# Optimization experiments

Hardware: AMD Instinct MI355X
Metric: run time of the kernel (lower is better)

## Reference

```python
import jax, jax.numpy as jnp
import numpy as np

D_MODEL = 256   # dim // 2
DIM = 512
D_INNER = 512   # expand=2 * d_model
D_STATE = 16
D_CONV = 4
DT_RANK = 16    # ceil(d_model/16)
N_LAYERS = 2
H_RES, W_RES = 16, 16
EPS = 1e-5


def silu(v):
    return v * jax.nn.sigmoid(v)


def setup_inputs() -> dict:
    key = jax.random.key(0)
    ks = jax.random.split(key, 12)
    Bsz, T, N = 2, 4, 256
    x = jax.random.normal(ks[0], (Bsz, 1 + T * N, DIM), jnp.float32)
    skip = jax.random.normal(ks[1], (Bsz, 1 + 4 * T * N, D_MODEL), jnp.float32)
    sc = lambda k, shape, s: jax.random.normal(k, shape, jnp.float32) * s
    exp_w = sc(ks[2], (2 * DIM, DIM), 0.02)            # PatchExpanding2D.expansion (no bias)
    ln_g = jnp.ones((DIM // 2,), jnp.float32)
    ln_b = jnp.zeros((DIM // 2,), jnp.float32)
    cls_w = sc(ks[3], (DIM // 2, DIM), 0.02)
    cls_b = jnp.zeros((DIM // 2,), jnp.float32)
    in_proj_w = sc(ks[4], (N_LAYERS, 2 * D_INNER, D_MODEL), 0.02)
    conv_w = sc(ks[5], (N_LAYERS, D_INNER, D_CONV), 0.1)  # depthwise causal conv
    conv_b = jnp.zeros((N_LAYERS, D_INNER), jnp.float32)
    xproj_w = sc(ks[6], (N_LAYERS, DT_RANK + 2 * D_STATE, D_INNER), 0.02)
    dt_w = sc(ks[7], (N_LAYERS, D_INNER, DT_RANK), 0.1)
    dt_b = sc(ks[8], (N_LAYERS, D_INNER), 0.1)
    A_log = jnp.log(jnp.broadcast_to(jnp.arange(1, D_STATE + 1, dtype=jnp.float32), (N_LAYERS, D_INNER, D_STATE)))
    Dp = jnp.ones((N_LAYERS, D_INNER), jnp.float32)
    out_w = sc(ks[9], (N_LAYERS, D_MODEL, D_INNER), 0.02)
    bn_g = jnp.ones((D_MODEL,), jnp.float32)
    bn_b = jnp.zeros((D_MODEL,), jnp.float32)
    return {"x": x, "skip_connection": skip, "exp_w": exp_w, "ln_g": ln_g, "ln_b": ln_b,
            "cls_w": cls_w, "cls_b": cls_b, "in_proj_w": in_proj_w, "conv_w": conv_w,
            "conv_b": conv_b, "xproj_w": xproj_w, "dt_w": dt_w, "dt_b": dt_b,
            "A_log": A_log, "Dp": Dp, "out_w": out_w, "bn_g": bn_g, "bn_b": bn_b,
            "B": 2, "T": 4, "N": 256}


def mamba_layer(u, Wi, cw, cb, Wx, Wdt, bdt, A_log, Dd, Wo):
    # u: [B, L, d_model]
    Bb, L, _ = u.shape
    xz = jnp.einsum('bld,ed->ble', u, Wi)            # [B, L, 2*d_inner]
    xi, z = jnp.split(xz, 2, axis=-1)
    # depthwise causal conv1d (pad left d_conv-1)
    xp = jnp.pad(xi, ((0, 0), (D_CONV - 1, 0), (0, 0)))
    xc = cb + sum(cw[:, k] * xp[:, k:k + L, :] for k in range(D_CONV))
    xi = silu(xc)
    dbc = jnp.einsum('bld,ed->ble', xi, Wx)          # [B, L, dt_rank + 2*d_state]
    dt = dbc[..., :DT_RANK]
    Bm = dbc[..., DT_RANK:DT_RANK + D_STATE]
    Cm = dbc[..., DT_RANK + D_STATE:]
    delta = jax.nn.softplus(jnp.einsum('blr,dr->bld', dt, Wdt) + bdt)  # [B, L, d_inner]
    A = -jnp.exp(A_log)                              # [d_inner, d_state]

    def step(h, inp):
        d_t, B_t, C_t, x_t = inp                     # [B,d], [B,n], [B,n], [B,d]
        h = h * jnp.exp(d_t[..., None] * A) + d_t[..., None] * B_t[:, None, :] * x_t[..., None]
        y = jnp.einsum('bdn,bn->bd', h, C_t)
        return h, y

    h0 = jnp.zeros((Bb, D_INNER, D_STATE), u.dtype)
    xs = (jnp.swapaxes(delta, 0, 1), jnp.swapaxes(Bm, 0, 1),
          jnp.swapaxes(Cm, 0, 1), jnp.swapaxes(xi, 0, 1))
    _, ys = jax.lax.scan(step, h0, xs)               # ys: [L, B, d_inner]
    y = jnp.swapaxes(ys, 0, 1) + xi * Dd
    y = y * silu(z)
    return jnp.einsum('bld,od->blo', y, Wo)          # [B, L, d_model]


def reference(x, skip_connection, exp_w, ln_g, ln_b, cls_w, cls_b, in_proj_w, conv_w,
              conv_b, xproj_w, dt_w, dt_b, A_log, Dp, out_w, bn_g, bn_b, B, T, N):
    cls = x[:B, :1, :]                               # [B, 1, dim]
    toks = x[:, 1:, :].reshape(x.shape[0], T, N, DIM)
    # patch expanding: Linear dim -> 2*dim, then 2x2 pixel shuffle, LayerNorm(dim//2)
    e = jnp.einsum('btnm,em->btne', toks, exp_w)     # [B, T, N, 2*dim]
    m = (2 * DIM) // 4                               # dim // 2
    e = e.reshape(-1, T, H_RES, W_RES, 2, 2, m)
    e = jnp.transpose(e, (0, 1, 2, 4, 3, 5, 6)).reshape(-1, T, 4 * N, m)
    mu = e.mean(-1, keepdims=True)
    var = e.var(-1, keepdims=True)
    e = (e - mu) / jnp.sqrt(var + EPS) * ln_g + ln_b
    e = e.reshape(e.shape[0], T * 4 * N, m)
    cls = jnp.einsum('bom,em->boe', cls, cls_w) + cls_b
    xx = jnp.concatenate([cls, e], axis=1) + skip_connection
    for i in range(N_LAYERS):
        xx = mamba_layer(xx, in_proj_w[i], conv_w[i], conv_b[i], xproj_w[i],
                         dt_w[i], dt_b[i], A_log[i], Dp[i], out_w[i])
    # BatchNorm1d over channels (training-mode batch stats, biased variance)
    mu = xx.mean(axis=(0, 1))
    var = xx.var(axis=(0, 1))
    xx = (xx - mu) / jnp.sqrt(var + EPS) * bn_g + bn_b
    return xx, 4 * N
```

## Files before the change

kernel.cpp:

```cpp
#include <hip/hip_runtime.h>
#include <hip/hip_bf16.h>
#include <math.h>

#define L_TOT 4097
#define BSZ 2
#define ROWS (BSZ*L_TOT)
#define NSEG 128
#define SEGLEN 33

typedef __bf16 bf16x8 __attribute__((ext_vector_type(8)));
typedef float  f32x4  __attribute__((ext_vector_type(4)));
#define ASTR 56

__device__ __forceinline__ float sigmoidf_(float v){ return 1.0f/(1.0f+__expf(-v)); }
__device__ __forceinline__ float siluf_(float v){ return v * sigmoidf_(v); }
__device__ __forceinline__ unsigned short bfbits(float f){
    __bf16 h = (__bf16)f;
    return __builtin_bit_cast(unsigned short, h);
}

__global__ __launch_bounds__(256) void cvt4(
    const float* __restrict__ w0, const float* __restrict__ w1,
    const float* __restrict__ w2, const float* __restrict__ w3,
    __bf16* __restrict__ o0, __bf16* __restrict__ o1,
    __bf16* __restrict__ o2, __bf16* __restrict__ o3)
{
    long i = ((long)blockIdx.x*256 + threadIdx.x)*8;
    const float* src; __bf16* dst; long off;
    if (i < 524288)        { src = w0; dst = o0; off = i; }
    else if (i < 1048576)  { src = w1; dst = o1; off = i - 524288; }
    else if (i < 1310720)  { src = w2; dst = o2; off = i - 1048576; }
    else if (i < 1359872)  { src = w3; dst = o3; off = i - 1310720; }
    else return;
    float4 a = *(const float4*)(src+off), b = *(const float4*)(src+off+4);
    bf16x8 o;
    o[0]=(__bf16)a.x; o[1]=(__bf16)a.y; o[2]=(__bf16)a.z; o[3]=(__bf16)a.w;
    o[4]=(__bf16)b.x; o[5]=(__bf16)b.y; o[6]=(__bf16)b.z; o[7]=(__bf16)b.w;
    *(bf16x8*)(dst+off) = o;
}

__global__ __launch_bounds__(256) void cvt_gather_x(
    const float* __restrict__ x, __bf16* __restrict__ out)
{
    long i = ((long)blockIdx.x*256 + threadIdx.x)*8;
    if (i >= 2048L*512) return;
    int row = (int)(i >> 9), col = (int)(i & 511);
    long srow = row + (row >> 10) + 1;
    const float* src = x + srow*512 + col;
    float4 a = *(const float4*)src, b = *(const float4*)(src+4);
    bf16x8 o;
    o[0]=(__bf16)a.x; o[1]=(__bf16)a.y; o[2]=(__bf16)a.z; o[3]=(__bf16)a.w;
    o[4]=(__bf16)b.x; o[5]=(__bf16)b.y; o[6]=(__bf16)b.z; o[7]=(__bf16)b.w;
    *(bf16x8*)(out+i) = o;
}

template<int SMODE>
__global__ __launch_bounds__(256) void gemm_bf16(
    const __bf16* __restrict__ A, const __bf16* __restrict__ W,
    float* __restrict__ C, __bf16* __restrict__ C2, int M, int N, int K)
{
    __shared__ __bf16 Als[128*ASTR];
    __shared__ __bf16 Wls[64*ASTR];
    const int tid = threadIdx.x;
    const int lane = tid & 63, w = tid >> 6;
    const int n0 = blockIdx.x*64, m0 = blockIdx.y*128;

    f32x4 zero = {0.f,0.f,0.f,0.f};
    f32x4 acc[2][4];
    #pragma unroll
    for (int i=0;i<2;i++)
        #pragma unroll
        for (int j=0;j<4;j++) acc[i][j] = zero;

    const int arow = tid >> 1, ahalf = tid & 1;
    const int wrow = tid >> 2, wseg = tid & 3;
    const int fr = lane & 15, fc = lane >> 4;

    for (int k0 = 0; k0 < K; k0 += 32) {
        bf16x8 av0 = {}, av1 = {};
        if (m0 + arow < M) {
            const __bf16* src = A + (long)(m0+arow)*K + k0 + ahalf*16;
            av0 = *(const bf16x8*)src;
            av1 = *(const bf16x8*)(src+8);
        }
        bf16x8 wv = *(const bf16x8*)(W + (long)(n0+wrow)*K + k0 + wseg*8);
        __syncthreads();
        *(bf16x8*)&Als[arow*ASTR + ahalf*16]     = av0;
        *(bf16x8*)&Als[arow*ASTR + ahalf*16 + 8] = av1;
        *(bf16x8*)&Wls[wrow*ASTR + wseg*8]       = wv;
        __syncthreads();

        bf16x8 a0 = *(const bf16x8*)&Als[(w*32 +      fr)*ASTR + fc*8];
        bf16x8 a1 = *(const bf16x8*)&Als[(w*32 + 16 + fr)*ASTR + fc*8];
        #pragma unroll
        for (int j = 0; j < 4; j++) {
            bf16x8 bv = *(const bf16x8*)&Wls[(j*16 + fr)*ASTR + fc*8];
            acc[0][j] = __builtin_amdgcn_mfma_f32_16x16x32_bf16(a0, bv, acc[0][j], 0,0,0);
            acc[1][j] = __builtin_amdgcn_mfma_f32_16x16x32_bf16(a1, bv, acc[1][j], 0,0,0);
        }
    }
    #pragma unroll
    for (int i = 0; i < 2; i++) {
        #pragma unroll
        for (int rr = 0; rr < 4; rr++) {
            int grow = m0 + w*32 + i*16 + fc*4 + rr;
            if (grow < M) {
                #pragma unroll
                for (int j = 0; j < 4; j++) {
                    float v = acc[i][j][rr];
                    long o = (long)grow*N + n0 + j*16 + fr;
                    if (SMODE != 2) C[o] = v;
                    if (SMODE != 0) C2[o] = (__bf16)v;
                }
            }
        }
    }
}

__global__ __launch_bounds__(128) void gemm_dbc(
    const __bf16* __restrict__ A, const __bf16* __restrict__ W,
    float* __restrict__ C, int M)
{
    __shared__ __bf16 Als[64*ASTR];
    __shared__ __bf16 Wls[48*ASTR];
    const int tid = threadIdx.x;
    const int lane = tid & 63, w = tid >> 6;
    const int m0 = blockIdx.x*64;
    f32x4 zero = {0.f,0.f,0.f,0.f};
    f32x4 acc[2][3];
    #pragma unroll
    for (int i=0;i<2;i++)
        #pragma unroll
        for (int j=0;j<3;j++) acc[i][j] = zero;

    const int arow = tid >> 1, ahalf = tid & 1;
    const int fr = lane & 15, fc = lane >> 4;

    for (int k0 = 0; k0 < 512; k0 += 32) {
        bf16x8 av0 = {}, av1 = {};
        if (m0 + arow < M) {
            const __bf16* src = A + (long)(m0+arow)*512 + k0 + ahalf*16;
            av0 = *(const bf16x8*)src;
            av1 = *(const bf16x8*)(src+8);
        }
        bf16x8 wv0 = {}, wv1 = {};
        if (tid < 96) {
            const __bf16* src = W + (long)(tid>>1)*512 + k0 + (tid&1)*16;
            wv0 = *(const bf16x8*)src;
            wv1 = *(const bf16x8*)(src+8);
        }
        __syncthreads();
        *(bf16x8*)&Als[arow*ASTR + ahalf*16]     = av0;
        *(bf16x8*)&Als[arow*ASTR + ahalf*16 + 8] = av1;
        if (tid < 96) {
            *(bf16x8*)&Wls[(tid>>1)*ASTR + (tid&1)*16]     = wv0;
            *(bf16x8*)&Wls[(tid>>1)*ASTR + (tid&1)*16 + 8] = wv1;
        }
        __syncthreads();

        bf16x8 a0 = *(const bf16x8*)&Als[(w*32 +      fr)*ASTR + fc*8];
        bf16x8 a1 = *(const bf16x8*)&Als[(w*32 + 16 + fr)*ASTR + fc*8];
        #pragma unroll
        for (int j = 0; j < 3; j++) {
            bf16x8 bv = *(const bf16x8*)&Wls[(j*16 + fr)*ASTR + fc*8];
            acc[0][j] = __builtin_amdgcn_mfma_f32_16x16x32_bf16(a0, bv, acc[0][j], 0,0,0);
            acc[1][j] = __builtin_amdgcn_mfma_f32_16x16x32_bf16(a1, bv, acc[1][j], 0,0,0);
        }
    }
    #pragma unroll
    for (int i = 0; i < 2; i++) {
        #pragma unroll
        for (int rr = 0; rr < 4; rr++) {
            int grow = m0 + w*32 + i*16 + fc*4 + rr;
            if (grow < M) {
                #pragma unroll
                for (int j = 0; j < 3; j++)
                    C[(long)grow*48 + j*16 + fr] = acc[i][j][rr];
            }
        }
    }
}

__global__ __launch_bounds__(256) void delta_k(
    const float* __restrict__ dbc, const float* __restrict__ Wdt,
    const float* __restrict__ bdt, const __bf16* __restrict__ xib,
    unsigned* __restrict__ pdx)
{
    const int d0 = threadIdx.x, d1 = threadIdx.x + 256;
    const int r0 = blockIdx.x*8;
    f32x4 wa[4], wb[4];
    #pragma unroll
    for (int q = 0; q < 4; q++) {
        wa[q] = *(const f32x4*)(Wdt + d0*16 + q*4);
        wb[q] = *(const f32x4*)(Wdt + d1*16 + q*4);
    }
    const float b0 = bdt[d0], b1 = bdt[d1];
    #pragma unroll
    for (int rr = 0; rr < 8; rr++) {
        int row = r0 + rr;
        if (row >= ROWS) return;
        const f32x4* p = (const f32x4*)(dbc + (long)row*48);
        f32x4 t0 = p[0], t1 = p[1], t2 = p[2], t3 = p[3];
        float s0 = b0, s1 = b1;
        #pragma unroll
        for (int e = 0; e < 4; e++) {
            s0 += wa[0][e]*t0[e] + wa[1][e]*t1[e] + wa[2][e]*t2[e] + wa[3][e]*t3[e];
            s1 += wb[0][e]*t0[e] + wb[1][e]*t1[e] + wb[2][e]*t2[e] + wb[3][e]*t3[e];
        }
        float dl0 = (s0 > 20.f) ? s0 : log1pf(__expf(s0));
        float dl1 = (s1 > 20.f) ? s1 : log1pf(__expf(s1));
        unsigned x0 = __builtin_bit_cast(unsigned short, xib[(long)row*512 + d0]);
        unsigned x1 = __builtin_bit_cast(unsigned short, xib[(long)row*512 + d1]);
        pdx[(long)row*512 + d0] = (unsigned)bfbits(dl0) | (x0 << 16);
        pdx[(long)row*512 + d1] = (unsigned)bfbits(dl1) | (x1 << 16);
    }
}

__global__ __launch_bounds__(256) void rearrange_ln_cls(
    const __bf16* __restrict__ e_buf, const float* __restrict__ x,
    const float* __restrict__ cls_w, const float* __restrict__ cls_b,
    const float* __restrict__ ln_g, const float* __restrict__ ln_b,
    const float* __restrict__ skip, float* __restrict__ xx,
    __bf16* __restrict__ xxb)
{
    const int blk = blockIdx.x;
    const int b = blk / L_TOT;
    const int q = blk % L_TOT;
    const int c = threadIdx.x;

    if (q == 0) {
        __shared__ float xr[512];
        const float* xrow = x + (long)b*1025*512;
        xr[c] = xrow[c]; xr[c+256] = xrow[c+256];
        __syncthreads();
        float acc = cls_b[c];
        const float4* wrow = (const float4*)(cls_w + (long)c*512);
        #pragma unroll 8
        for (int m4 = 0; m4 < 128; m4++) {
            float4 wv = wrow[m4];
            float4 xv = *(const float4*)&xr[m4*4];
            acc += wv.x*xv.x + wv.y*xv.y + wv.z*xv.z + wv.w*xv.w;
        }
        long o = (long)b*L_TOT*256 + c;
        float v = acc + skip[o];
        xx[o] = v; xxb[o] = (__bf16)v;
        return;
    }
    const int t  = (q-1) >> 10;
    const int p  = (q-1) & 1023;
    const int h  = p >> 6;
    const int a  = (p >> 5) & 1;
    const int w  = (p >> 1) & 15;
    const int bb = p & 1;
    const long tok = (long)b*1024 + t*256 + h*16 + w;
    float v = (float)e_buf[tok*1024 + a*512 + bb*256 + c];

    float s = v, s2 = v*v;
    #pragma unroll
    for (int o = 32; o > 0; o >>= 1) { s += __shfl_xor(s, o); s2 += __shfl_xor(s2, o); }
    __shared__ float ps[4], ps2[4];
    __shared__ float mu_s, rs_s;
    const int wv = threadIdx.x >> 6;
    if ((threadIdx.x & 63) == 0) { ps[wv] = s; ps2[wv] = s2; }
    __syncthreads();
    if (threadIdx.x == 0) {
        float S = ps[0]+ps[1]+ps[2]+ps[3];
        float S2 = ps2[0]+ps2[1]+ps2[2]+ps2[3];
        float mu = S * (1.f/256.f);
        float var = S2 * (1.f/256.f) - mu*mu;
        mu_s = mu; rs_s = rsqrtf(var + 1e-5f);
    }
    __syncthreads();
    long o = ((long)b*L_TOT + q)*256 + c;
    float outv = (v - mu_s)*rs_s*ln_g[c] + ln_b[c] + skip[o];
    xx[o] = outv; xxb[o] = (__bf16)outv;
}

__global__ __launch_bounds__(256) void conv_silu_split(
    const __bf16* __restrict__ xzb, const float* __restrict__ cw,
    const float* __restrict__ cb, __bf16* __restrict__ xib,
    __bf16* __restrict__ zsb)
{
    long tid = (long)blockIdx.x*256 + threadIdx.x;
    if (tid >= (long)ROWS*128) return;
    int chunk = (int)(tid & 127);
    long rl = tid >> 7;
    if (chunk < 64) {
        int d0 = chunk*8;
        int l = (int)(rl % L_TOT);
        float acc[8];
        #pragma unroll
        for (int e = 0; e < 8; e++) acc[e] = cb[d0+e];
        #pragma unroll
        for (int k = 0; k < 4; k++) {
            int ls = l + k - 3;
            if (ls >= 0) {
                bf16x8 v = *(const bf16x8*)&xzb[(rl + (k-3))*1024 + d0];
                #pragma unroll
                for (int e = 0; e < 8; e++)
                    acc[e] += cw[(d0+e)*4 + k] * (float)v[e];
            }
        }
        bf16x8 o;
        #pragma unroll
        for (int e = 0; e < 8; e++) o[e] = (__bf16)siluf_(acc[e]);
        *(bf16x8*)&xib[rl*512 + d0] = o;
    } else {
        int d0 = (chunk - 64)*8;
        bf16x8 v = *(const bf16x8*)&xzb[rl*1024 + 512 + d0];
        bf16x8 o;
        #pragma unroll
        for (int e = 0; e < 8; e++) o[e] = (__bf16)siluf_((float)v[e]);
        *(bf16x8*)&zsb[rl*512 + d0] = o;
    }
}

__global__ __launch_bounds__(256) void scan_p1(
    const unsigned* __restrict__ pdx,
    const float* __restrict__ dbc, const float* __restrict__ A_log,
    float* __restrict__ segH, float* __restrict__ segP)
{
    const int seg = blockIdx.x >> 4;
    const int t = ((blockIdx.x & 15) << 8) + threadIdx.x;
    const int b = t >> 11;
    const int d = (t >> 2) & 511;
    const int ng = t & 3;
    f32x4 Al = *(const f32x4*)(A_log + d*16 + ng*4);
    float Ar[4] = {-__expf(Al[0]), -__expf(Al[1]), -__expf(Al[2]), -__expf(Al[3])};
    float h[4] = {0,0,0,0};
    float P[4] = {1,1,1,1};
    const int l0 = seg*SEGLEN;
    const int l1 = min(l0 + SEGLEN, L_TOT);
    for (int l = l0; l < l1; l++) {
        long base = (long)b*L_TOT + l;
        unsigned v = pdx[base*512 + d];
        float dl = __uint_as_float(v << 16);
        float xv = __uint_as_float(v & 0xffff0000u);
        f32x4 Bv = *(const f32x4*)(dbc + base*48 + 16 + ng*4);
        float dx = dl*xv;
        #pragma unroll
        for (int n = 0; n < 4; n++) {
            float E = __expf(dl*Ar[n]);
            h[n] = h[n]*E + dx*Bv[n];
            P[n] *= E;
        }
    }
    long off = ((long)(seg*2 + b)*512 + d)*16 + ng*4;
    *(f32x4*)&segH[off] = f32x4{h[0],h[1],h[2],h[3]};
    *(f32x4*)&segP[off] = f32x4{P[0],P[1],P[2],P[3]};
}

__global__ __launch_bounds__(256) void scan_p2(
    float* __restrict__ segH, const float* __restrict__ segP)
{
    const int idx = blockIdx.x*256 + threadIdx.x;
    float carry = 0.f;
    for (int s0 = 0; s0 < NSEG; s0 += 8) {
        float hh[8], pp[8];
        #pragma unroll
        for (int j = 0; j < 8; j++) {
            long o = (long)(s0+j)*16384 + idx;
            hh[j] = segH[o]; pp[j] = segP[o];
        }
        #pragma unroll
        for (int j = 0; j < 8; j++) {
            long o = (long)(s0+j)*16384 + idx;
            segH[o] = carry;
            carry = pp[j]*carry + hh[j];
        }
    }
}

__global__ __launch_bounds__(256) void scan_p3(
    const unsigned* __restrict__ pdx,
    const float* __restrict__ dbc, const float* __restrict__ A_log,
    const float* __restrict__ segH, const float* __restrict__ Dp,
    const __bf16* __restrict__ zsb, __bf16* __restrict__ yb)
{
    const int seg = blockIdx.x >> 4;
    const int t = ((blockIdx.x & 15) << 8) + threadIdx.x;
    const int b = t >> 11;
    const int d = (t >> 2) & 511;
    const int ng = t & 3;
    f32x4 Al = *(const f32x4*)(A_log + d*16 + ng*4);
    float Ar[4] = {-__expf(Al[0]), -__expf(Al[1]), -__expf(Al[2]), -__expf(Al[3])};
    long off = ((long)(seg*2 + b)*512 + d)*16 + ng*4;
    f32x4 h4 = *(const f32x4*)&segH[off];
    float h[4] = {h4[0], h4[1], h4[2], h4[3]};
    const float Dd = Dp[d];
    const int l0 = seg*SEGLEN;
    const int l1 = min(l0 + SEGLEN, L_TOT);
    for (int l = l0; l < l1; l++) {
        long base = (long)b*L_TOT + l;
        unsigned v = pdx[base*512 + d];
        float dl = __uint_as_float(v << 16);
        float xv = __uint_as_float(v & 0xffff0000u);
        f32x4 Bv = *(const f32x4*)(dbc + base*48 + 16 + ng*4);
        f32x4 Cv = *(const f32x4*)(dbc + base*48 + 32 + ng*4);
        float dx = dl*xv;
        float y = 0.f;
        #pragma unroll
        for (int n = 0; n < 4; n++) {
            float E = __expf(dl*Ar[n]);
            h[n] = h[n]*E + dx*Bv[n];
            y += h[n]*Cv[n];
        }
        y += __shfl_xor(y, 1);
        y += __shfl_xor(y, 2);
        if (ng == 0) {
            float z = (float)zsb[base*512 + d];
            float yo = (y + xv*Dd) * z;
            yb[base*512 + d] = (__bf16)yo;
        }
    }
}

__global__ void zero_stats(float* __restrict__ stats) { stats[threadIdx.x] = 0.f; }

__global__ __launch_bounds__(256) void bn_reduce(
    const float* __restrict__ xx, float* __restrict__ stats)
{
    const int c = threadIdx.x;
    float s = 0.f, s2 = 0.f;
    for (int r = blockIdx.x; r < ROWS; r += gridDim.x) {
        float v = xx[(long)r*256 + c];
        s += v; s2 += v*v;
    }
    atomicAdd(&stats[c], s);
    atomicAdd(&stats[256 + c], s2);
}

__global__ __launch_bounds__(256) void bn_apply(
    const float* __restrict__ xx, const float* __restrict__ stats,
    const float* __restrict__ g, const float* __restrict__ bta,
    float* __restrict__ out)
{
    long idx = (long)blockIdx.x*256 + threadIdx.x;
    if (idx == 0) out[(long)ROWS*256] = 1024.0f;
    if (idx >= (long)ROWS*256) return;
    int c = (int)(idx & 255);
    float mu = stats[c] * (1.f/ROWS);
    float var = stats[256 + c] * (1.f/ROWS) - mu*mu;
    out[idx] = (xx[idx] - mu)*rsqrtf(var + 1e-5f)*g[c] + bta[c];
}

extern "C" void kernel_launch(void* const* d_in, const int* in_sizes, int n_in,
                              void* d_out, int out_size, void* d_ws, size_t ws_size,
                              hipStream_t stream)
{
    const float* x        = (const float*)d_in[0];
    const float* skip     = (const float*)d_in[1];
    const float* exp_w    = (const float*)d_in[2];
    const float* ln_g     = (const float*)d_in[3];
    const float* ln_b     = (const float*)d_in[4];
    const float* cls_w    = (const float*)d_in[5];
    const float* cls_b    = (const float*)d_in[6];
    const float* in_proj_w= (const float*)d_in[7];
    const float* conv_w   = (const float*)d_in[8];
    const float* conv_b   = (const float*)d_in[9];
    const float* xproj_w  = (const float*)d_in[10];
    const float* dt_w     = (const float*)d_in[11];
    const float* dt_b     = (const float*)d_in[12];
    const float* A_log    = (const float*)d_in[13];
    const float* Dp       = (const float*)d_in[14];
    const float* out_w    = (const float*)d_in[15];
    const float* bn_g     = (const float*)d_in[16];
    const float* bn_b     = (const float*)d_in[17];

    float* ws = (float*)d_ws;
    float* xx    = ws;
    float* dbc   = xx + 2097664;
    float* segH  = dbc + 393312;
    float* segP  = segH + 2097152;
    float* stats = segP + 2097152;
    unsigned* pdx = (unsigned*)(stats + 512);
    __bf16* expWb = (__bf16*)(pdx + 4195328);
    __bf16* inWb  = expWb + 524288;
    __bf16* outWb = inWb + 524288;
    __bf16* xpWb  = outWb + 262144;
    __bf16* xxb   = xpWb + 49152;
    __bf16* xzb   = xxb + 2097664;
    __bf16* e_b   = xzb;
    __bf16* xib   = xzb + 8390656;
    __bf16* Axb   = xib;
    __bf16* zsb   = xib + 4195328;
    __bf16* yb    = zsb + 4195328;
    float* out    = (float*)d_out;

    cvt4<<<(1359872/8 + 255)/256, 256, 0, stream>>>(
        exp_w, in_proj_w, out_w, xproj_w, expWb, inWb, outWb, xpWb);
    cvt_gather_x<<<(1048576/8)/256, 256, 0, stream>>>(x, Axb);

    gemm_bf16<2><<<dim3(16, 16), 256, 0, stream>>>(
        Axb, expWb, nullptr, e_b, 2048, 1024, 512);
    rearrange_ln_cls<<<ROWS, 256, 0, stream>>>(
        e_b, x, cls_w, cls_b, ln_g, ln_b, skip, xx, xxb);

    for (int layer = 0; layer < 2; layer++) {
        gemm_bf16<2><<<dim3(16, 65), 256, 0, stream>>>(
            xxb, inWb + layer*262144, nullptr, xzb, ROWS, 1024, 256);
        conv_silu_split<<<((long)ROWS*128 + 255)/256, 256, 0, stream>>>(
            xzb, conv_w + layer*512*4, conv_b + layer*512, xib, zsb);
        gemm_dbc<<<(ROWS + 63)/64, 128, 0, stream>>>(
            xib, xpWb + layer*24576, dbc, ROWS);
        delta_k<<<(ROWS + 7)/8, 256, 0, stream>>>(
            dbc, dt_w + layer*512*16, dt_b + layer*512, xib, pdx);
        scan_p1<<<NSEG*16, 256, 0, stream>>>(
            pdx, dbc, A_log + layer*512*16, segH, segP);
        scan_p2<<<64, 256, 0, stream>>>(segH, segP);
        scan_p3<<<NSEG*16, 256, 0, stream>>>(
            pdx, dbc, A_log + layer*512*16, segH, Dp + layer*512, zsb, yb);
        if (layer == 0) {
            gemm_bf16<1><<<dim3(4, 65), 256, 0, stream>>>(
                yb, outWb, xx, xxb, ROWS, 256, 512);
        } else {
            gemm_bf16<0><<<dim3(4, 65), 256, 0, stream>>>(
                yb, outWb + 131072, xx, nullptr, ROWS, 256, 512);
        }
    }

    zero_stats<<<1, 512, 0, stream>>>(stats);
    bn_reduce<<<128, 256, 0, stream>>>(xx, stats);
    bn_apply<<<((long)ROWS*256 + 255)/256 + 1, 256, 0, stream>>>(xx, stats, bn_g, bn_b, out);
}
```

Before: 466.9 us.

## Add 128x128 in_proj GEMM, sliding-window conv, and LDS-staged scan kernels

Adds a 128x128-tile bf16 MFMA GEMM with a K-step of 64 for the in_proj projection. The depthwise conv now handles 8 rows per thread, keeping a register sliding window and conv weights in registers. Both scan passes now stage pdx, B/C and z for a segment into shared memory with coalesced vector loads. The output pass also writes y back through shared memory in coalesced vectors. These target redundant global loads and uncoalesced per-element scan accesses, at the cost of more registers and LDS, which may lower occupancy.

```diff
diff --git a/kernel.cpp b/kernel.cpp
--- a/kernel.cpp
+++ b/kernel.cpp
@@ -11,6 +11,7 @@
 typedef __bf16 bf16x8 __attribute__((ext_vector_type(8)));
 typedef float  f32x4  __attribute__((ext_vector_type(4)));
 #define ASTR 56
+#define AST2 72
 
 __device__ __forceinline__ float sigmoidf_(float v){ return 1.0f/(1.0f+__expf(-v)); }
 __device__ __forceinline__ float siluf_(float v){ return v * sigmoidf_(v); }
@@ -65,13 +66,7 @@
     const int lane = tid & 63, w = tid >> 6;
     const int n0 = blockIdx.x*64, m0 = blockIdx.y*128;
 
-    f32x4 zero = {0.f,0.f,0.f,0.f};
-    f32x4 acc[2][4];
-    #pragma unroll
-    for (int i=0;i<2;i++)
-        #pragma unroll
-        for (int j=0;j<4;j++) acc[i][j] = zero;
-
+    f32x4 acc[2][4] = {};
     const int arow = tid >> 1, ahalf = tid & 1;
     const int wrow = tid >> 2, wseg = tid & 3;
     const int fr = lane & 15, fc = lane >> 4;
@@ -117,6 +112,63 @@
     }
 }
 
+__global__ __launch_bounds__(256) void gemm_bf16_128(
+    const __bf16* __restrict__ A, const __bf16* __restrict__ W,
+    __bf16* __restrict__ C2, int M, int N, int K)
+{
+    __shared__ __bf16 Als[128*AST2];
+    __shared__ __bf16 Wls[128*AST2];
+    const int tid = threadIdx.x;
+    const int lane = tid & 63, w = tid >> 6;
+    const int n0 = blockIdx.x*128, m0 = blockIdx.y*128;
+    const int fr = lane & 15, fc = lane >> 4;
+    const int row2 = tid >> 1, half = tid & 1;
+
+    f32x4 acc[2][8] = {};
+
+    for (int k0 = 0; k0 < K; k0 += 64) {
+        bf16x8 av[4], wv[4];
+        const bool aok = (m0 + row2) < M;
+        const __bf16* asrc = A + (long)(m0+row2)*K + k0 + half*32;
+        const __bf16* wsrc = W + (long)(n0+row2)*K + k0 + half*32;
+        #pragma unroll
+        for (int e = 0; e < 4; e++) {
+            av[e] = aok ? *(const bf16x8*)(asrc + e*8) : (bf16x8){};
+            wv[e] = *(const bf16x8*)(wsrc + e*8);
+        }
+        __syncthreads();
+        #pragma unroll
+        for (int e = 0; e < 4; e++) {
+            *(bf16x8*)&Als[row2*AST2 + half*32 + e*8] = av[e];
+            *(bf16x8*)&Wls[row2*AST2 + half*32 + e*8] = wv[e];
+        }
+        __syncthreads();
+        #pragma unroll
+        for (int s = 0; s < 2; s++) {
+            bf16x8 a0 = *(const bf16x8*)&Als[(w*32 +      fr)*AST2 + s*32 + fc*8];
+            bf16x8 a1 = *(const bf16x8*)&Als[(w*32 + 16 + fr)*AST2 + s*32 + fc*8];
+            #pragma unroll
+            for (int j = 0; j < 8; j++) {
+                bf16x8 bv = *(const bf16x8*)&Wls[(j*16 + fr)*AST2 + s*32 + fc*8];
+                acc[0][j] = __builtin_amdgcn_mfma_f32_16x16x32_bf16(a0, bv, acc[0][j], 0,0,0);
+                acc[1][j] = __builtin_amdgcn_mfma_f32_16x16x32_bf16(a1, bv, acc[1][j], 0,0,0);
+            }
+        }
+    }
+    #pragma unroll
+    for (int i = 0; i < 2; i++) {
+        #pragma unroll
+        for (int rr = 0; rr < 4; rr++) {
+            int grow = m0 + w*32 + i*16 + fc*4 + rr;
+            if (grow < M) {
+                #pragma unroll
+                for (int j = 0; j < 8; j++)
+                    C2[(long)grow*N + n0 + j*16 + fr] = (__bf16)acc[i][j][rr];
+            }
+        }
+    }
+}
+
 __global__ __launch_bounds__(128) void gemm_dbc(
     const __bf16* __restrict__ A, const __bf16* __restrict__ W,
     float* __restrict__ C, int M)
@@ -126,12 +178,7 @@
     const int tid = threadIdx.x;
     const int lane = tid & 63, w = tid >> 6;
     const int m0 = blockIdx.x*64;
-    f32x4 zero = {0.f,0.f,0.f,0.f};
-    f32x4 acc[2][3];
-    #pragma unroll
-    for (int i=0;i<2;i++)
-        #pragma unroll
-        for (int j=0;j<3;j++) acc[i][j] = zero;
+    f32x4 acc[2][3] = {};
 
     const int arow = tid >> 1, ahalf = tid & 1;
     const int fr = lane & 15, fc = lane >> 4;
@@ -281,37 +328,61 @@
     const float* __restrict__ cb, __bf16* __restrict__ xib,
     __bf16* __restrict__ zsb)
 {
-    long tid = (long)blockIdx.x*256 + threadIdx.x;
-    if (tid >= (long)ROWS*128) return;
-    int chunk = (int)(tid & 127);
-    long rl = tid >> 7;
-    if (chunk < 64) {
-        int d0 = chunk*8;
-        int l = (int)(rl % L_TOT);
-        float acc[8];
-        #pragma unroll
-        for (int e = 0; e < 8; e++) acc[e] = cb[d0+e];
-        #pragma unroll
-        for (int k = 0; k < 4; k++) {
-            int ls = l + k - 3;
-            if (ls >= 0) {
-                bf16x8 v = *(const bf16x8*)&xzb[(rl + (k-3))*1024 + d0];
-                #pragma unroll
-                for (int e = 0; e < 8; e++)
-                    acc[e] += cw[(d0+e)*4 + k] * (float)v[e];
+    const int tid = threadIdx.x;
+    const int c = tid & 127;
+    const long r0 = ((long)blockIdx.x*2 + (tid >> 7))*8;
+    if (r0 >= ROWS) return;
+
+    if (c < 64) {
+        const int d0 = c*8;
+        float wreg[4][8], breg[8];
+        #pragma unroll
+        for (int e = 0; e < 8; e++) {
+            breg[e] = cb[d0+e];
+            #pragma unroll
+            for (int k = 0; k < 4; k++) wreg[k][e] = cw[(d0+e)*4 + k];
+        }
+        bf16x8 win[4];
+        #pragma unroll
+        for (int j = 0; j < 3; j++) {
+            long rr = r0 - 3 + j;
+            win[j] = (rr >= 0) ? *(const bf16x8*)&xzb[rr*1024 + d0] : (bf16x8){};
+        }
+        #pragma unroll
+        for (int rr = 0; rr < 8; rr++) {
+            long rl = r0 + rr;
+            if (rl >= ROWS) break;
+            win[3] = *(const bf16x8*)&xzb[rl*1024 + d0];
+            int l = (int)(rl % L_TOT);
+            float acc[8];
+            #pragma unroll
+            for (int e = 0; e < 8; e++) acc[e] = breg[e];
+            #pragma unroll
+            for (int k = 0; k < 4; k++) {
+                if (l + k - 3 >= 0) {
+                    #pragma unroll
+                    for (int e = 0; e < 8; e++)
+                        acc[e] += wreg[k][e]*(float)win[k][e];
+                }
             }
-        }
-        bf16x8 o;
-        #pragma unroll
-        for (int e = 0; e < 8; e++) o[e] = (__bf16)siluf_(acc[e]);
-        *(bf16x8*)&xib[rl*512 + d0] = o;
+            bf16x8 o;
+            #pragma unroll
+            for (int e = 0; e < 8; e++) o[e] = (__bf16)siluf_(acc[e]);
+            *(bf16x8*)&xib[rl*512 + d0] = o;
+            win[0] = win[1]; win[1] = win[2]; win[2] = win[3];
+        }
     } else {
-        int d0 = (chunk - 64)*8;
-        bf16x8 v = *(const bf16x8*)&xzb[rl*1024 + 512 + d0];
-        bf16x8 o;
-        #pragma unroll
-        for (int e = 0; e < 8; e++) o[e] = (__bf16)siluf_((float)v[e]);
-        *(bf16x8*)&zsb[rl*512 + d0] = o;
+        const int d0 = (c - 64)*8;
+        #pragma unroll
+        for (int rr = 0; rr < 8; rr++) {
+            long rl = r0 + rr;
+            if (rl >= ROWS) break;
+            bf16x8 v = *(const bf16x8*)&xzb[rl*1024 + 512 + d0];
+            bf16x8 o;
+            #pragma unroll
+            for (int e = 0; e < 8; e++) o[e] = (__bf16)siluf_((float)v[e]);
+            *(bf16x8*)&zsb[rl*512 + d0] = o;
+        }
     }
 }
 
@@ -320,23 +391,41 @@
     const float* __restrict__ dbc, const float* __restrict__ A_log,
     float* __restrict__ segH, float* __restrict__ segP)
 {
-    const int seg = blockIdx.x >> 4;
-    const int t = ((blockIdx.x & 15) << 8) + threadIdx.x;
-    const int b = t >> 11;
-    const int d = (t >> 2) & 511;
-    const int ng = t & 3;
+    __shared__ unsigned pdxS[SEGLEN*64];
+    __shared__ float bS[SEGLEN*16];
+    const int blk = blockIdx.x;
+    const int seg = blk >> 4;
+    const int b   = (blk >> 3) & 1;
+    const int dbase = (blk & 7)*64;
+    const int tid = threadIdx.x;
+    const int l0 = seg*SEGLEN;
+    const int nl = min(l0 + SEGLEN, L_TOT) - l0;
+    const int nlc = nl > 0 ? nl : 0;
+
+    for (int cc = tid; cc < nlc*16; cc += 256) {
+        int l = cc >> 4, qq = cc & 15;
+        *(uint4*)&pdxS[l*64 + qq*4] =
+            *(const uint4*)&pdx[((long)b*L_TOT + l0 + l)*512 + dbase + qq*4];
+    }
+    for (int cc = tid; cc < nlc*4; cc += 256) {
+        int l = cc >> 2, qq = cc & 3;
+        *(f32x4*)&bS[l*16 + qq*4] =
+            *(const f32x4*)&dbc[((long)b*L_TOT + l0 + l)*48 + 16 + qq*4];
+    }
+    __syncthreads();
+
+    const int dl_ = tid >> 2;
+    const int d = dbase + dl_;
+    const int ng = tid & 3;
     f32x4 Al = *(const f32x4*)(A_log + d*16 + ng*4);
     float Ar[4] = {-__expf(Al[0]), -__expf(Al[1]), -__expf(Al[2]), -__expf(Al[3])};
     float h[4] = {0,0,0,0};
     float P[4] = {1,1,1,1};
-    const int l0 = seg*SEGLEN;
-    const int l1 = min(l0 + SEGLEN, L_TOT);
-    for (int l = l0; l < l1; l++) {
-        long base = (long)b*L_TOT + l;
-        unsigned v = pdx[base*512 + d];
+    for (int l = 0; l < nlc; l++) {
+        unsigned v = pdxS[l*64 + dl_];
         float dl = __uint_as_float(v << 16);
         float xv = __uint_as_float(v & 0xffff0000u);
-        f32x4 Bv = *(const f32x4*)(dbc + base*48 + 16 + ng*4);
+        f32x4 Bv = *(const f32x4*)&bS[l*16 + ng*4];
         float dx = dl*xv;
         #pragma unroll
         for (int n = 0; n < 4; n++) {
@@ -377,26 +466,52 @@
     const float* __restrict__ segH, const float* __restrict__ Dp,
     const __bf16* __restrict__ zsb, __bf16* __restrict__ yb)
 {
-    const int seg = blockIdx.x >> 4;
-    const int t = ((blockIdx.x & 15) << 8) + threadIdx.x;
-    const int b = t >> 11;
-    const int d = (t >> 2) & 511;
-    const int ng = t & 3;
+    __shared__ unsigned pdxS[SEGLEN*64];
+    __shared__ float bcS[SEGLEN*32];
+    __shared__ __bf16 zS[SEGLEN*64];
+    __shared__ __bf16 yS[SEGLEN*64];
+    const int blk = blockIdx.x;
+    const int seg = blk >> 4;
+    const int b   = (blk >> 3) & 1;
+    const int dbase = (blk & 7)*64;
+    const int tid = threadIdx.x;
+    const int l0 = seg*SEGLEN;
+    const int nl = min(l0 + SEGLEN, L_TOT) - l0;
+    const int nlc = nl > 0 ? nl : 0;
+    if (nlc == 0) return;
+
+    for (int cc = tid; cc < nlc*16; cc += 256) {
+        int l = cc >> 4, qq = cc & 15;
+        *(uint4*)&pdxS[l*64 + qq*4] =
+            *(const uint4*)&pdx[((long)b*L_TOT + l0 + l)*512 + dbase + qq*4];
+    }
+    for (int cc = tid; cc < nlc*8; cc += 256) {
+        int l = cc >> 3, qq = cc & 7;
+        *(f32x4*)&bcS[l*32 + qq*4] =
+            *(const f32x4*)&dbc[((long)b*L_TOT + l0 + l)*48 + 16 + qq*4];
+    }
+    for (int cc = tid; cc < nlc*8; cc += 256) {
+        int l = cc >> 3, qq = cc & 7;
+        *(bf16x8*)&zS[l*64 + qq*8] =
+            *(const bf16x8*)&zsb[((long)b*L_TOT + l0 + l)*512 + dbase + qq*8];
+    }
+    __syncthreads();
+
+    const int dl_ = tid >> 2;
+    const int d = dbase + dl_;
+    const int ng = tid & 3;
     f32x4 Al = *(const f32x4*)(A_log + d*16 + ng*4);
     float Ar[4] = {-__expf(Al[0]), -__expf(Al[1]), -__expf(Al[2]), -__expf(Al[3])};
     long off = ((long)(seg*2 + b)*512 + d)*16 + ng*4;
     f32x4 h4 = *(const f32x4*)&segH[off];
     float h[4] = {h4[0], h4[1], h4[2], h4[3]};
     const float Dd = Dp[d];
-    const int l0 = seg*SEGLEN;
-    const int l1 = min(l0 + SEGLEN, L_TOT);
-    for (int l = l0; l < l1; l++) {
-        long base = (long)b*L_TOT + l;
-        unsigned v = pdx[base*512 + d];
+    for (int l = 0; l < nlc; l++) {
+        unsigned v = pdxS[l*64 + dl_];
         float dl = __uint_as_float(v << 16);
         float xv = __uint_as_float(v & 0xffff0000u);
-        f32x4 Bv = *(const f32x4*)(dbc + base*48 + 16 + ng*4);
-        f32x4 Cv = *(const f32x4*)(dbc + base*48 + 32 + ng*4);
+        f32x4 Bv = *(const f32x4*)&bcS[l*32 + ng*4];
+        f32x4 Cv = *(const f32x4*)&bcS[l*32 + 16 + ng*4];
         float dx = dl*xv;
         float y = 0.f;
         #pragma unroll
@@ -408,10 +523,15 @@
         y += __shfl_xor(y, 1);
         y += __shfl_xor(y, 2);
         if (ng == 0) {
-            float z = (float)zsb[base*512 + d];
-            float yo = (y + xv*Dd) * z;
-            yb[base*512 + d] = (__bf16)yo;
-        }
+            float z = (float)zS[l*64 + dl_];
+            yS[l*64 + dl_] = (__bf16)((y + xv*Dd)*z);
+        }
+    }
+    __syncthreads();
+    for (int cc = tid; cc < nlc*8; cc += 256) {
+        int l = cc >> 3, qq = cc & 7;
+        *(bf16x8*)&yb[((long)b*L_TOT + l0 + l)*512 + dbase + qq*8] =
+            *(bf16x8*)&yS[l*64 + qq*8];
     }
 }
 
@@ -497,9 +617,9 @@
         e_b, x, cls_w, cls_b, ln_g, ln_b, skip, xx, xxb);
 
     for (int layer = 0; layer < 2; layer++) {
-        gemm_bf16<2><<<dim3(16, 65), 256, 0, stream>>>(
-            xxb, inWb + layer*262144, nullptr, xzb, ROWS, 1024, 256);
-        conv_silu_split<<<((long)ROWS*128 + 255)/256, 256, 0, stream>>>(
+        gemm_bf16_128<<<dim3(8, 65), 256, 0, stream>>>(
+            xxb, inWb + layer*262144, xzb, ROWS, 1024, 256);
+        conv_silu_split<<<513, 256, 0, stream>>>(
             xzb, conv_w + layer*512*4, conv_b + layer*512, xib, zsb);
         gemm_dbc<<<(ROWS + 63)/64, 128, 0, stream>>>(
             xib, xpWb + layer*24576, dbc, ROWS);
```

Result: faster. 406.9 us (-12.8%).
